# Kernel tuning notes

Measured on AMD Instinct MI355X. Metric: run time of the kernel, lower is better.

The kernel has to match this reference:

```python
import jax, jax.numpy as jnp
import numpy as np

V, E, H = 32000, 50, 100
B, T = 8, 512


def setup_inputs() -> dict:
    key = jax.random.key(0)
    ks = jax.random.split(key, 12)
    inputs = jax.random.randint(ks[0], (B, T), 0, V, dtype=jnp.int64)
    d = {
        "inputs": inputs,
        "embedding": jax.random.normal(ks[1], (V, E), jnp.float32),
        "W_hr": jax.random.normal(ks[2], (H, H), jnp.float32) * 0.01,
        "W_xr": jax.random.normal(ks[3], (E, H), jnp.float32) * 0.01,
        "b_r": jnp.zeros((H,), jnp.float32),
        "W_hz": jax.random.normal(ks[4], (H, H), jnp.float32) * 0.01,
        "W_xz": jax.random.normal(ks[5], (E, H), jnp.float32) * 0.01,
        "b_z": jnp.zeros((H,), jnp.float32),
        "W_hh": jax.random.normal(ks[6], (H, H), jnp.float32) * 0.01,
        "W_xh": jax.random.normal(ks[7], (E, H), jnp.float32) * 0.01,
        "b_h": jnp.zeros((H,), jnp.float32),
        "fc_W": jax.random.normal(ks[8], (H, V), jnp.float32) * 0.01,
        "fc_b": jnp.zeros((V,), jnp.float32),
    }
    return d


def reference(inputs, embedding, W_hr, W_xr, b_r, W_hz, W_xz, b_z,
              W_hh, W_xh, b_h, fc_W, fc_b):
    # Embed all timesteps at once: [B, T, E] -> time-major [T, B, E]
    x = embedding[inputs]
    x_tm = jnp.transpose(x, (1, 0, 2))

    h0 = jnp.zeros((inputs.shape[0], W_hr.shape[0]), dtype=embedding.dtype)

    def step(h_t, x_t):
        R_t = jax.nn.sigmoid(h_t @ W_hr + x_t @ W_xr + b_r)
        Z_t = jax.nn.sigmoid(h_t @ W_hz + x_t @ W_xz + b_z)
        # NOTE: original torch code computes (R_t * h_t) @ W_hh (left-to-right precedence)
        h_tilda = jnp.tanh((R_t * h_t) @ W_hh + x_t @ W_xh + b_h)
        h_new = Z_t * h_tilda + (1.0 - Z_t) * h_t
        y_t = h_new @ fc_W + fc_b  # [B, V]
        return h_new, y_t

    _, ys = jax.lax.scan(step, h0, x_tm)  # ys: [T, B, V]
    return jnp.transpose(ys, (1, 0, 2))   # [B, T, V]
```

## Files before the change

### kernel.cpp

```cpp
#include <hip/hip_runtime.h>
#include <hip/hip_bf16.h>
#include <hip/hip_fp16.h>
#include <math.h>

#define NV 32000
#define NE 50
#define NH 100
#define NB 8
#define NT 512
#define CH 8
#define KP 112

typedef __attribute__((ext_vector_type(8)))  _Float16 f16x8;
typedef __attribute__((ext_vector_type(16))) float    f32x16;

__device__ __forceinline__ void bar_lgkm() {
    __builtin_amdgcn_sched_barrier(0);
    asm volatile("s_waitcnt lgkmcnt(0)" ::: "memory");
    __builtin_amdgcn_s_barrier();
    asm volatile("" ::: "memory");
    __builtin_amdgcn_sched_barrier(0);
}

__global__ __launch_bounds__(256) void convw_kernel(
    const float* __restrict__ W, _Float16* __restrict__ Wp)
{
    int wv = threadIdx.x >> 6, l = threadIdx.x & 63;
    int ct = blockIdx.x * 4 + wv;
    int v  = ct * 32 + (l & 31);
    int kb = (l >> 5) * 8;
    _Float16* dst = Wp + (size_t)ct * 7 * 512 + l * 8;
    for (int kt = 0; kt < 7; kt++) {
        f16x8 tmp;
        #pragma unroll
        for (int j = 0; j < 8; j++) {
            int k = kt * 16 + kb + j;
            tmp[j] = (_Float16)(k < NH ? W[(size_t)k * NV + v] : 0.0f);
        }
        *(f16x8*)(dst + (size_t)kt * 512) = tmp;
    }
}

__global__ __launch_bounds__(128) void xproj_kernel(
    const int* __restrict__ inp, const float* __restrict__ emb,
    const float* __restrict__ Wxr, const float* __restrict__ br,
    const float* __restrict__ Wxz, const float* __restrict__ bz,
    const float* __restrict__ Wxh, const float* __restrict__ bh,
    float* __restrict__ Xr, float* __restrict__ Xz, float* __restrict__ Xh)
{
    int n = blockIdx.x;
    int t = n >> 3, b = n & 7;
    __shared__ float xs[NE];
    int tid = threadIdx.x;
    int idx = inp[b * NT + t];
    if (tid < NE) xs[tid] = emb[idx * NE + tid];
    __syncthreads();
    if (tid < NH) {
        float ar = br[tid], az = bz[tid], ah = bh[tid];
        for (int e = 0; e < NE; e++) {
            float x = xs[e];
            ar += x * Wxr[e * NH + tid];
            az += x * Wxz[e * NH + tid];
            ah += x * Wxh[e * NH + tid];
        }
        Xr[n * NH + tid] = ar;
        Xz[n * NH + tid] = az;
        Xh[n * NH + tid] = ah;
    }
}

__global__ __launch_bounds__(768, 3) void gru_rec_kernel(
    const float* __restrict__ Whr, const float* __restrict__ Whz,
    const float* __restrict__ Whh,
    const float* __restrict__ Xr, const float* __restrict__ Xz,
    const float* __restrict__ Xh, _Float16* __restrict__ Hp)
{
    int b   = blockIdx.x;
    int tid = threadIdx.x;
    int g   = tid >> 8;
    int u   = tid & 255;
    int q   = u >> 6;
    int l   = u & 63;
    int jj  = q * 32 + (l & 31);
    int kh  = l >> 5;
    int kbase = kh * 52;
    int jc  = (jj < NH) ? jj : 0;
    bool act = (kh == 0) && (jj < NH);

    __shared__ __align__(16) float h_s[104];
    __shared__ __align__(16) float rh_s[104];
    __shared__ __align__(16) float z_s[104];

    const float* W  = (g == 0) ? Whr : (g == 1) ? Whz : Whh;
    const float* Xg = (g == 0) ? Xr  : (g == 1) ? Xz  : Xh;

    float w[52];
    #pragma unroll
    for (int m = 0; m < 52; m++) {
        int k = kbase + m;
        w[m] = (jj < NH && k < NH) ? W[k * NH + jj] : 0.0f;
    }
    if (tid < 104) { h_s[tid] = 0.0f; rh_s[tid] = 0.0f; z_s[tid] = 0.0f; }
    __syncthreads();

    float xb_cur[CH], xb_nxt[CH];
    if (act) {
        #pragma unroll
        for (int i = 0; i < CH; i++)
            xb_cur[i] = Xg[(i * NB + b) * NH + jj];
    }

    for (int tc = 0; tc < NT; tc += CH) {
        if (act && tc + CH < NT) {
            #pragma unroll
            for (int i = 0; i < CH; i++)
                xb_nxt[i] = Xg[((tc + CH + i) * NB + b) * NH + jj];
        }
        #pragma unroll
        for (int i = 0; i < CH; i++) {
            int t = tc + i;
            if (g < 2) {
                float hj = h_s[jc];
                float a0 = 0.f, a1 = 0.f, a2 = 0.f, a3 = 0.f;
                const float4* hv4 = (const float4*)h_s + kh * 13;
                #pragma unroll
                for (int kk = 0; kk < 13; kk++) {
                    float4 hv = hv4[kk];
                    a0 += hv.x * w[4 * kk + 0];
                    a1 += hv.y * w[4 * kk + 1];
                    a2 += hv.z * w[4 * kk + 2];
                    a3 += hv.w * w[4 * kk + 3];
                }
                float part = (a0 + a1) + (a2 + a3);
                float tot  = part + __shfl_xor(part, 32, 64);
                if (act) {
                    float s = 1.0f / (1.0f + __expf(-(tot + xb_cur[i])));
                    if (g == 0) rh_s[jj] = s * hj;
                    else        z_s[jj]  = s;
                }
            }
            bar_lgkm();
            if (g == 2) {
                float a0 = 0.f, a1 = 0.f, a2 = 0.f, a3 = 0.f;
                const float4* rv4 = (const float4*)rh_s + kh * 13;
                #pragma unroll
                for (int kk = 0; kk < 13; kk++) {
                    float4 rv = rv4[kk];
                    a0 += rv.x * w[4 * kk + 0];
                    a1 += rv.y * w[4 * kk + 1];
                    a2 += rv.z * w[4 * kk + 2];
                    a3 += rv.w * w[4 * kk + 3];
                }
                float part = (a0 + a1) + (a2 + a3);
                float tot  = part + __shfl_xor(part, 32, 64);
                if (act) {
                    float a  = tot + xb_cur[i];
                    float e  = __expf(2.0f * a);
                    float ht = 1.0f - 2.0f / (e + 1.0f);
                    float z  = z_s[jc], h = h_s[jc];
                    float hn = fmaf(z, ht - h, h);
                    h_s[jj] = hn;
                    size_t n2 = (size_t)(t * NB + b) * KP;
                    Hp[n2 + jj] = (_Float16)hn;
                    if (jj < KP - NH) Hp[n2 + NH + jj] = (_Float16)0.0f;
                }
            }
            bar_lgkm();
        }
        if (act) {
            #pragma unroll
            for (int i = 0; i < CH; i++) xb_cur[i] = xb_nxt[i];
        }
    }
}

__global__ __launch_bounds__(256) void outgemm_kernel(
    const _Float16* __restrict__ Hp, const _Float16* __restrict__ Wp,
    const float* __restrict__ fcb, float* __restrict__ out)
{
    int tid = threadIdx.x;
    int wv = tid >> 6, l = tid & 63;
    int n0 = blockIdx.x * 32;
    int cb = blockIdx.y * 256 + wv * 64;

    const _Float16* arow = Hp + (size_t)(n0 + (l & 31)) * KP + (l >> 5) * 8;
    f16x8 a[7];
    #pragma unroll
    for (int kt = 0; kt < 7; kt++)
        a[kt] = *(const f16x8*)(arow + kt * 16);

    int ct0 = cb >> 5;
    const _Float16* bp = Wp + (size_t)ct0 * 7 * 512 + l * 8;

    f32x16 acc0 = {0,0,0,0,0,0,0,0,0,0,0,0,0,0,0,0};
    f32x16 acc1 = {0,0,0,0,0,0,0,0,0,0,0,0,0,0,0,0};
    #pragma unroll
    for (int kt = 0; kt < 7; kt++) {
        f16x8 b0 = *(const f16x8*)(bp + (size_t)kt * 512);
        f16x8 b1 = *(const f16x8*)(bp + (size_t)(kt + 7) * 512);
        acc0 = __builtin_amdgcn_mfma_f32_32x32x16_f16(a[kt], b0, acc0, 0, 0, 0);
        acc1 = __builtin_amdgcn_mfma_f32_32x32x16_f16(a[kt], b1, acc1, 0, 0, 0);
    }

    int c0 = cb + (l & 31);
    float bias0 = fcb[c0], bias1 = fcb[c0 + 32];
    #pragma unroll
    for (int p = 0; p < 16; p++) {
        int r = (p & 3) + 8 * (p >> 2) + 4 * (l >> 5);
        int m = n0 + r;
        size_t row = (size_t)(m & 7) * NT + (m >> 3);
        out[row * NV + c0]      = acc0[p] + bias0;
        out[row * NV + c0 + 32] = acc1[p] + bias1;
    }
}

extern "C" void kernel_launch(void* const* d_in, const int* in_sizes, int n_in,
                              void* d_out, int out_size, void* d_ws, size_t ws_size,
                              hipStream_t stream)
{
    const int*   inp = (const int*)  d_in[0];
    const float* emb = (const float*)d_in[1];
    const float* Whr = (const float*)d_in[2];
    const float* Wxr = (const float*)d_in[3];
    const float* br  = (const float*)d_in[4];
    const float* Whz = (const float*)d_in[5];
    const float* Wxz = (const float*)d_in[6];
    const float* bz  = (const float*)d_in[7];
    const float* Whh = (const float*)d_in[8];
    const float* Wxh = (const float*)d_in[9];
    const float* bh  = (const float*)d_in[10];
    const float* fcW = (const float*)d_in[11];
    const float* fcb = (const float*)d_in[12];
    float* out = (float*)d_out;

    float*    Xr = (float*)d_ws;
    float*    Xz = Xr + NT * NB * NH;
    float*    Xh = Xz + NT * NB * NH;
    _Float16* Hp = (_Float16*)(Xh + NT * NB * NH);
    _Float16* Wp = Hp + (size_t)NT * NB * KP;

    convw_kernel<<<NV / 32 / 4, 256, 0, stream>>>(fcW, Wp);
    xproj_kernel<<<NT * NB, 128, 0, stream>>>(inp, emb, Wxr, br, Wxz, bz, Wxh, bh,
                                              Xr, Xz, Xh);
    gru_rec_kernel<<<NB, 768, 0, stream>>>(Whr, Whz, Whh, Xr, Xz, Xh, Hp);
    dim3 ggrid(NT * NB / 32, NV / 256);
    outgemm_kernel<<<ggrid, 256, 0, stream>>>(Hp, Wp, fcb, out);
}
```

Before: 611.2 us.

## Run GRU recurrence matmuls on MFMA with fp16 hidden state in LDS

Replaces the scalar FMA recurrence kernel, which used 768 threads and per-thread fp32 weight registers, with a 256-thread kernel. Each wave holds fp16 MFMA B-fragments of the three hidden-weight matrices and computes the gate projections with 16x16x32 MFMAs. A new small kernel pre-packs the hidden weights into fragment layout. The hidden state and R*h are kept as fp16 in LDS, and the X-projections are prefetched one step ahead instead of in chunks. The aim is to shorten the serial per-timestep latency, at the cost of fp16 rounding of the recurrent state and wasted MFMA rows, since only one of the 16 rows holds real data.

```diff
diff --git a/kernel.cpp b/kernel.cpp
--- a/kernel.cpp
+++ b/kernel.cpp
@@ -8,10 +8,11 @@
 #define NH 100
 #define NB 8
 #define NT 512
-#define CH 8
 #define KP 112
+#define HS 136
 
 typedef __attribute__((ext_vector_type(8)))  _Float16 f16x8;
+typedef __attribute__((ext_vector_type(4)))  float    f32x4;
 typedef __attribute__((ext_vector_type(16))) float    f32x16;
 
 __device__ __forceinline__ void bar_lgkm() {
@@ -39,6 +40,25 @@
         }
         *(f16x8*)(dst + (size_t)kt * 512) = tmp;
     }
+}
+
+__global__ __launch_bounds__(64) void convg_kernel(
+    const float* __restrict__ Whr, const float* __restrict__ Whz,
+    const float* __restrict__ Whh, _Float16* __restrict__ Wg)
+{
+    int f = blockIdx.x;
+    int g = f / 28, rem = f % 28, n = rem / 4, kt = rem % 4;
+    const float* W = (g == 0) ? Whr : (g == 1) ? Whz : Whh;
+    int l   = threadIdx.x;
+    int col = n * 16 + (l & 15);
+    int k0  = kt * 32 + (l >> 4) * 8;
+    f16x8 v;
+    #pragma unroll
+    for (int j = 0; j < 8; j++) {
+        int k = k0 + j;
+        v[j] = (_Float16)((k < NH && col < NH) ? W[k * NH + col] : 0.0f);
+    }
+    *(f16x8*)(Wg + (size_t)f * 512 + l * 8) = v;
 }
 
 __global__ __launch_bounds__(128) void xproj_kernel(
@@ -69,108 +89,113 @@
     }
 }
 
-__global__ __launch_bounds__(768, 3) void gru_rec_kernel(
-    const float* __restrict__ Whr, const float* __restrict__ Whz,
-    const float* __restrict__ Whh,
+__global__ __launch_bounds__(256) void gru_rec_kernel(
+    const _Float16* __restrict__ Wg,
     const float* __restrict__ Xr, const float* __restrict__ Xz,
     const float* __restrict__ Xh, _Float16* __restrict__ Hp)
 {
     int b   = blockIdx.x;
     int tid = threadIdx.x;
-    int g   = tid >> 8;
-    int u   = tid & 255;
-    int q   = u >> 6;
-    int l   = u & 63;
-    int jj  = q * 32 + (l & 31);
-    int kh  = l >> 5;
-    int kbase = kh * 52;
-    int jc  = (jj < NH) ? jj : 0;
-    bool act = (kh == 0) && (jj < NH);
-
-    __shared__ __align__(16) float h_s[104];
-    __shared__ __align__(16) float rh_s[104];
-    __shared__ __align__(16) float z_s[104];
-
-    const float* W  = (g == 0) ? Whr : (g == 1) ? Whz : Whh;
-    const float* Xg = (g == 0) ? Xr  : (g == 1) ? Xz  : Xh;
-
-    float w[52];
-    #pragma unroll
-    for (int m = 0; m < 52; m++) {
-        int k = kbase + m;
-        w[m] = (jj < NH && k < NH) ? W[k * NH + jj] : 0.0f;
-    }
-    if (tid < 104) { h_s[tid] = 0.0f; rh_s[tid] = 0.0f; z_s[tid] = 0.0f; }
+    int w   = tid >> 6, l = tid & 63;
+    int lj  = l & 15;
+
+    __shared__ __align__(16) _Float16 h16[16 * HS];
+    __shared__ __align__(16) _Float16 rh16[16 * HS];
+    for (int i = tid; i < 16 * HS; i += 256) { h16[i] = (_Float16)0.0f; rh16[i] = (_Float16)0.0f; }
     __syncthreads();
 
-    float xb_cur[CH], xb_nxt[CH];
-    if (act) {
+    int n0 = w, n1 = w + 4;
+    bool has1 = (n1 < 7);
+    int n1c = has1 ? n1 : n0;
+
+    f16x8 WR0[4], WZ0[4], WH0[4], WR1[4], WZ1[4], WH1[4];
+    #pragma unroll
+    for (int kt = 0; kt < 4; kt++) {
+        WR0[kt] = *(const f16x8*)(Wg + (size_t)(((0*7 + n0)*4 + kt))*512 + l*8);
+        WZ0[kt] = *(const f16x8*)(Wg + (size_t)(((1*7 + n0)*4 + kt))*512 + l*8);
+        WH0[kt] = *(const f16x8*)(Wg + (size_t)(((2*7 + n0)*4 + kt))*512 + l*8);
+        WR1[kt] = *(const f16x8*)(Wg + (size_t)(((0*7 + n1c)*4 + kt))*512 + l*8);
+        WZ1[kt] = *(const f16x8*)(Wg + (size_t)(((1*7 + n1c)*4 + kt))*512 + l*8);
+        WH1[kt] = *(const f16x8*)(Wg + (size_t)(((2*7 + n1c)*4 + kt))*512 + l*8);
+    }
+
+    int j0 = n0 * 16 + lj;
+    int j1 = n1c * 16 + lj;
+    int j0x = j0 < NH ? j0 : NH - 1;
+    int j1x = j1 < NH ? j1 : NH - 1;
+
+    float h0 = 0.0f, h1 = 0.0f;
+    float xr0, xz0, xh0, xr1, xz1, xh1;
+    if (l < 16) {
+        int base = b * NH;
+        xr0 = Xr[base + j0x]; xz0 = Xz[base + j0x]; xh0 = Xh[base + j0x];
+        xr1 = Xr[base + j1x]; xz1 = Xz[base + j1x]; xh1 = Xh[base + j1x];
+    }
+
+    int aoff = lj * HS + (l >> 4) * 8;
+
+    for (int t = 0; t < NT; t++) {
+        float pr0, pz0, ph0, pr1, pz1, ph1;
+        if (l < 16 && t + 1 < NT) {
+            int base = ((t + 1) * NB + b) * NH;
+            pr0 = Xr[base + j0x]; pz0 = Xz[base + j0x]; ph0 = Xh[base + j0x];
+            pr1 = Xr[base + j1x]; pz1 = Xz[base + j1x]; ph1 = Xh[base + j1x];
+        }
+
+        f32x4 aR0 = {0,0,0,0}, aZ0 = {0,0,0,0}, aR1 = {0,0,0,0}, aZ1 = {0,0,0,0};
         #pragma unroll
-        for (int i = 0; i < CH; i++)
-            xb_cur[i] = Xg[(i * NB + b) * NH + jj];
-    }
-
-    for (int tc = 0; tc < NT; tc += CH) {
-        if (act && tc + CH < NT) {
-            #pragma unroll
-            for (int i = 0; i < CH; i++)
-                xb_nxt[i] = Xg[((tc + CH + i) * NB + b) * NH + jj];
-        }
+        for (int kt = 0; kt < 4; kt++) {
+            f16x8 a = *(const f16x8*)&h16[aoff + kt * 32];
+            aR0 = __builtin_amdgcn_mfma_f32_16x16x32_f16(a, WR0[kt], aR0, 0, 0, 0);
+            aZ0 = __builtin_amdgcn_mfma_f32_16x16x32_f16(a, WZ0[kt], aZ0, 0, 0, 0);
+            aR1 = __builtin_amdgcn_mfma_f32_16x16x32_f16(a, WR1[kt], aR1, 0, 0, 0);
+            aZ1 = __builtin_amdgcn_mfma_f32_16x16x32_f16(a, WZ1[kt], aZ1, 0, 0, 0);
+        }
+        float z0 = 0.0f, z1 = 0.0f;
+        if (l < 16) {
+            float r0 = 1.0f / (1.0f + __expf(-(aR0[0] + xr0)));
+            z0       = 1.0f / (1.0f + __expf(-(aZ0[0] + xz0)));
+            rh16[j0] = (_Float16)(j0 < NH ? r0 * h0 : 0.0f);
+            if (has1) {
+                float r1 = 1.0f / (1.0f + __expf(-(aR1[0] + xr1)));
+                z1       = 1.0f / (1.0f + __expf(-(aZ1[0] + xz1)));
+                rh16[j1] = (_Float16)(j1 < NH ? r1 * h1 : 0.0f);
+            }
+        }
+        bar_lgkm();
+
+        f32x4 aH0 = {0,0,0,0}, aH1 = {0,0,0,0};
         #pragma unroll
-        for (int i = 0; i < CH; i++) {
-            int t = tc + i;
-            if (g < 2) {
-                float hj = h_s[jc];
-                float a0 = 0.f, a1 = 0.f, a2 = 0.f, a3 = 0.f;
-                const float4* hv4 = (const float4*)h_s + kh * 13;
-                #pragma unroll
-                for (int kk = 0; kk < 13; kk++) {
-                    float4 hv = hv4[kk];
-                    a0 += hv.x * w[4 * kk + 0];
-                    a1 += hv.y * w[4 * kk + 1];
-                    a2 += hv.z * w[4 * kk + 2];
-                    a3 += hv.w * w[4 * kk + 3];
-                }
-                float part = (a0 + a1) + (a2 + a3);
-                float tot  = part + __shfl_xor(part, 32, 64);
-                if (act) {
-                    float s = 1.0f / (1.0f + __expf(-(tot + xb_cur[i])));
-                    if (g == 0) rh_s[jj] = s * hj;
-                    else        z_s[jj]  = s;
-                }
+        for (int kt = 0; kt < 4; kt++) {
+            f16x8 a = *(const f16x8*)&rh16[aoff + kt * 32];
+            aH0 = __builtin_amdgcn_mfma_f32_16x16x32_f16(a, WH0[kt], aH0, 0, 0, 0);
+            aH1 = __builtin_amdgcn_mfma_f32_16x16x32_f16(a, WH1[kt], aH1, 0, 0, 0);
+        }
+        if (l < 16) {
+            size_t hpb = (size_t)(t * NB + b) * KP;
+            {
+                float e  = __expf(2.0f * (aH0[0] + xh0));
+                float ht = 1.0f - 2.0f / (e + 1.0f);
+                float hn = fmaf(z0, ht - h0, h0);
+                hn = (j0 < NH) ? hn : 0.0f;
+                h0 = hn;
+                h16[j0] = (_Float16)hn;
+                Hp[hpb + j0] = (_Float16)hn;
             }
-            bar_lgkm();
-            if (g == 2) {
-                float a0 = 0.f, a1 = 0.f, a2 = 0.f, a3 = 0.f;
-                const float4* rv4 = (const float4*)rh_s + kh * 13;
-                #pragma unroll
-                for (int kk = 0; kk < 13; kk++) {
-                    float4 rv = rv4[kk];
-                    a0 += rv.x * w[4 * kk + 0];
-                    a1 += rv.y * w[4 * kk + 1];
-                    a2 += rv.z * w[4 * kk + 2];
-                    a3 += rv.w * w[4 * kk + 3];
-                }
-                float part = (a0 + a1) + (a2 + a3);
-                float tot  = part + __shfl_xor(part, 32, 64);
-                if (act) {
-                    float a  = tot + xb_cur[i];
-                    float e  = __expf(2.0f * a);
-                    float ht = 1.0f - 2.0f / (e + 1.0f);
-                    float z  = z_s[jc], h = h_s[jc];
-                    float hn = fmaf(z, ht - h, h);
-                    h_s[jj] = hn;
-                    size_t n2 = (size_t)(t * NB + b) * KP;
-                    Hp[n2 + jj] = (_Float16)hn;
-                    if (jj < KP - NH) Hp[n2 + NH + jj] = (_Float16)0.0f;
-                }
+            if (has1) {
+                float e  = __expf(2.0f * (aH1[0] + xh1));
+                float ht = 1.0f - 2.0f / (e + 1.0f);
+                float hn = fmaf(z1, ht - h1, h1);
+                hn = (j1 < NH) ? hn : 0.0f;
+                h1 = hn;
+                h16[j1] = (_Float16)hn;
+                Hp[hpb + j1] = (_Float16)hn;
             }
-            bar_lgkm();
-        }
-        if (act) {
-            #pragma unroll
-            for (int i = 0; i < CH; i++) xb_cur[i] = xb_nxt[i];
-        }
+        }
+        bar_lgkm();
+
+        xr0 = pr0; xz0 = pz0; xh0 = ph0;
+        xr1 = pr1; xz1 = pz1; xh1 = ph1;
     }
 }
 
@@ -238,11 +263,13 @@
     float*    Xh = Xz + NT * NB * NH;
     _Float16* Hp = (_Float16*)(Xh + NT * NB * NH);
     _Float16* Wp = Hp + (size_t)NT * NB * KP;
+    _Float16* Wg = Wp + (size_t)1000 * 7 * 512;
 
     convw_kernel<<<NV / 32 / 4, 256, 0, stream>>>(fcW, Wp);
+    convg_kernel<<<84, 64, 0, stream>>>(Whr, Whz, Whh, Wg);
     xproj_kernel<<<NT * NB, 128, 0, stream>>>(inp, emb, Wxr, br, Wxz, bz, Wxh, bh,
                                               Xr, Xz, Xh);
-    gru_rec_kernel<<<NB, 768, 0, stream>>>(Whr, Whz, Whh, Xr, Xz, Xh, Hp);
+    gru_rec_kernel<<<NB, 256, 0, stream>>>(Wg, Xr, Xz, Xh, Hp);
     dim3 ggrid(NT * NB / 32, NV / 256);
     outgemm_kernel<<<ggrid, 256, 0, stream>>>(Hp, Wp, fcb, out);
 }
```

Result: slower. 636.8 us (+4.2%).
